# Kernel optimization log

Measured on AMD Instinct MI355X. Metric: run time of the kernel, lower is better.

## Reference

```python
import jax, jax.numpy as jnp
import numpy as np

N = 4096          # rank / n
OFF_DIAG = 4      # banded half-width
D_IN = 4096       # v: [N, D_IN]
D_OUT = 4096      # u: [D_OUT, N]
BATCH, SEQ = 4, 2048


def _banded_indices(n, off_diag):
    """All (row, col) entries of the 2*off_diag+1 diagonals, like torch.sparse.spdiags."""
    rows, cols = [], []
    for off in range(-off_diag, off_diag + 1):
        if off >= 0:
            i = np.arange(0, n - off)
        else:
            i = np.arange(-off, n)
        rows.append(i)
        cols.append(i + off)
    return np.concatenate(rows).astype(np.int32), np.concatenate(cols).astype(np.int32)


def setup_inputs() -> dict:
    key = jax.random.key(0)
    k_x, k_u, k_v, k_sp, k_s = jax.random.split(key, 5)
    row, col = _banded_indices(N, OFF_DIAG)
    nnz = row.shape[0]  # 36844
    return {
        "x": jax.random.normal(k_x, (BATCH, SEQ, D_IN), dtype=jnp.float32),
        "u": jax.random.normal(k_u, (D_OUT, N), dtype=jnp.float32),
        "v": jax.random.normal(k_v, (N, D_IN), dtype=jnp.float32),
        "s_pre": jax.random.uniform(k_sp, (N,), dtype=jnp.float32),  # singular values (diag)
        # kaiming_normal_ on a [1, nnz] tensor -> std = sqrt(2 / nnz)
        "s": jax.random.normal(k_s, (nnz,), dtype=jnp.float32) * np.float32(np.sqrt(2.0 / nnz)),
        "gate": jnp.zeros((1,), dtype=jnp.float32),
        "row": jnp.asarray(row),
        "col": jnp.asarray(col),
    }


def reference(x, u, v, s_pre, s, gate, row, col):
    n = s_pre.shape[0]
    # del_s = diag(s_pre) + scatter(s * sigmoid(gate)) at banded indices  -> [n, n]
    vals = s * jax.nn.sigmoid(gate)          # [nnz]
    M = jnp.zeros((n, n), dtype=x.dtype).at[row, col].add(vals)
    M = M.at[jnp.arange(n), jnp.arange(n)].add(s_pre)
    # weight = ((del_s @ v).T) @ u.T  -> [D_IN, D_OUT]
    weight = (M @ v).T @ u.T
    return x @ weight
```

## Files before the change

kernel.cpp:

```cpp
#include <hip/hip_runtime.h>
#include <cstdint>

typedef unsigned short u16;
typedef __attribute__((ext_vector_type(8))) __bf16 bf16x8;
typedef __attribute__((ext_vector_type(4))) float f32x4;

#define N_DIM 4096

__device__ __forceinline__ u16 f2bf(float f) {
    union { float f; unsigned u; } c; c.f = f;
    unsigned u = c.u;
    u += 0x7FFFu + ((u >> 16) & 1u);
    return (u16)(u >> 16);
}

__device__ __forceinline__ void gl_lds16(const u16* g, u16* l) {
    __builtin_amdgcn_global_load_lds(
        (const __attribute__((address_space(1))) void*)g,
        (__attribute__((address_space(3))) void*)l, 16, 0, 0);
}

__global__ void band_kernel(const float* __restrict__ s,
                            const float* __restrict__ s_pre,
                            const float* __restrict__ gate,
                            float* __restrict__ bnd) {
    int n = blockIdx.x * blockDim.x + threadIdx.x;
    if (n >= N_DIM) return;
    float sig = 1.0f / (1.0f + __expf(-gate[0]));
    const int base[9] = {0, 4092, 8185, 12279, 16374, 20470, 24565, 28659, 32752};
    #pragma unroll
    for (int o = 0; o < 9; ++o) {
        int off = o - 4;
        int col = n + off;
        float val = 0.0f;
        if (col >= 0 && col < N_DIM) {
            int idx = (off >= 0) ? (base[o] + n) : (base[o] + n + off);
            val = s[idx] * sig;
        }
        if (off == 0) val += s_pre[n];
        bnd[n * 9 + o] = val;
    }
}

__global__ void band_combine_t(const float* __restrict__ v,
                               const float* __restrict__ bnd,
                               u16* __restrict__ P) {
    __shared__ float tile[32][33];
    int n0 = blockIdx.x * 32;
    int d0 = blockIdx.y * 32;
    int tx = threadIdx.x;
    int ty = threadIdx.y;
    #pragma unroll
    for (int i = 0; i < 4; ++i) {
        int nl = ty + 8 * i;
        int n = n0 + nl;
        int d = d0 + tx;
        float acc = 0.0f;
        #pragma unroll
        for (int o = 0; o < 9; ++o) {
            int src = n + o - 4;
            float w = bnd[n * 9 + o];
            float vv = ((unsigned)src < (unsigned)N_DIM) ? v[(size_t)src * N_DIM + d] : 0.0f;
            acc += w * vv;
        }
        tile[nl][tx] = acc;
    }
    __syncthreads();
    #pragma unroll
    for (int i = 0; i < 4; ++i) {
        int dl = ty + 8 * i;
        P[(size_t)(d0 + dl) * N_DIM + (n0 + tx)] = f2bf(tile[tx][dl]);
    }
}

__global__ void cvt_bf16(const float* __restrict__ in, u16* __restrict__ out, int nElem4) {
    int i = blockIdx.x * blockDim.x + threadIdx.x;
    if (i >= nElem4) return;
    float4 f = ((const float4*)in)[i];
    ushort4 o;
    o.x = f2bf(f.x); o.y = f2bf(f.y); o.z = f2bf(f.z); o.w = f2bf(f.w);
    ((ushort4*)out)[i] = o;
}

#define BARRIER() __builtin_amdgcn_s_barrier()
#define LGKM0()   asm volatile("s_waitcnt lgkmcnt(0)" ::: "memory")
#define VMC(n)    asm volatile("s_waitcnt vmcnt(" #n ")" ::: "memory")

#define MFMA_Q(QM, QN) do {                                                   \
    __builtin_amdgcn_s_setprio(1);                                            \
    _Pragma("unroll")                                                         \
    for (int k_ = 0; k_ < 2; ++k_)                                            \
      _Pragma("unroll")                                                       \
      for (int i_ = 0; i_ < 4; ++i_)                                          \
        _Pragma("unroll")                                                     \
        for (int j_ = 0; j_ < 2; ++j_)                                        \
          acc[(QM)*4 + i_][(QN)*2 + j_] =                                     \
            __builtin_amdgcn_mfma_f32_16x16x32_bf16(                          \
              aR[i_][k_], bR[(QN)*2 + j_][k_],                                \
              acc[(QM)*4 + i_][(QN)*2 + j_], 0, 0, 0);                        \
    __builtin_amdgcn_s_setprio(0);                                            \
  } while (0)

template <bool OUT_BF16>
__global__ __launch_bounds__(512, 2)
void gemm_tn8(const u16* __restrict__ A, const u16* __restrict__ B,
              float* __restrict__ Cf, u16* __restrict__ Cb,
              int M, int N, int K) {
    __shared__ __align__(16) u16 As[2][16384];
    __shared__ __align__(16) u16 Bs[2][16384];

    const int tid = threadIdx.x;
    const int l   = tid & 63;
    const int w   = tid >> 6;
    const int wm  = w >> 2;
    const int wn  = w & 3;

    const int nbx = gridDim.x;
    const int nwg = nbx * gridDim.y;
    int lid = blockIdx.y * nbx + blockIdx.x;
    if ((nwg & 7) == 0) lid = (lid & 7) * (nwg >> 3) + (lid >> 3);
    const long m0 = (long)(lid / nbx) * 256;
    const long n0 = (long)(lid % nbx) * 256;

    const u16* Ab = A + m0 * (long)K;
    const u16* Bb = B + n0 * (long)K;

    const int lin16 = (l < 32) ? l : (l ^ 2);
    const int sr = lin16 >> 2;
    const int sc = (lin16 & 3) * 8;
    const int s0 = w;
    const int s1 = 8 + w;
    const int g0 = ((s0 >> 1) * 16 + sr) * K + (s0 & 1) * 32 + sc;
    const int g1 = ((s1 >> 1) * 16 + sr) * K + (s1 & 1) * 32 + sc;
    const int d0 = s0 * 512 + l * 8;
    const int d1 = s1 * 512 + l * 8;

    const int foff = (((((l & 15) << 6) + ((l >> 4) << 4)) ^ (((l >> 3) & 1) << 5)) >> 1);
    const int abase = wm * 8192;
    const int bbase = wn * 4096;

    f32x4 acc[8][4];
    #pragma unroll
    for (int i = 0; i < 8; ++i)
        #pragma unroll
        for (int j = 0; j < 4; ++j)
            acc[i][j] = (f32x4){0.f, 0.f, 0.f, 0.f};

    bf16x8 aR[4][2], bR[4][2];

    auto stageA = [&](int buf, int t, int h) {
        const u16* g = Ab + (long)h * 128 * K + (long)t * 64;
        u16* lb = &As[buf][h * 8192];
        gl_lds16(g + g0, lb + d0);
        gl_lds16(g + g1, lb + d1);
    };
    auto stageB = [&](int buf, int t, int h) {
        const u16* g = Bb + (long)h * 128 * K + (long)t * 64;
        u16* lb = &Bs[buf][h * 8192];
        gl_lds16(g + g0, lb + d0);
        gl_lds16(g + g1, lb + d1);
    };
    auto loadA4 = [&](int buf, int fmBase) {
        #pragma unroll
        for (int i = 0; i < 4; ++i)
            #pragma unroll
            for (int ks = 0; ks < 2; ++ks)
                aR[i][ks] = *(const bf16x8*)&As[buf][abase + (fmBase + i) * 1024 + ks * 512 + foff];
    };
    auto loadB2 = [&](int buf, int fnBase) {
        #pragma unroll
        for (int i = 0; i < 2; ++i)
            #pragma unroll
            for (int ks = 0; ks < 2; ++ks)
                bR[fnBase + i][ks] = *(const bf16x8*)&Bs[buf][bbase + (fnBase + i) * 1024 + ks * 512 + foff];
    };

    const int NT = K >> 6;

    stageA(0, 0, 0); stageA(0, 0, 1);
    stageB(0, 0, 0); stageB(0, 0, 1);
    stageB(1, 1, 0); stageB(1, 1, 1);
    VMC(4);
    BARRIER();

    for (int it = 0; it < (NT >> 1); ++it) {
        const int kt = it * 2;
        const int t2 = (kt + 2 < NT) ? kt + 2 : NT - 1;
        const int t3 = (kt + 3 < NT) ? kt + 3 : NT - 1;

        loadA4(0, 0); loadB2(0, 0);
        stageA(1, kt + 1, 0);
        BARRIER(); LGKM0();
        MFMA_Q(0, 0);
        BARRIER();

        loadB2(0, 2);
        stageA(1, kt + 1, 1);
        BARRIER(); LGKM0();
        MFMA_Q(0, 1);
        BARRIER();

        loadA4(0, 4);
        stageB(0, t2, 0);
        BARRIER(); LGKM0();
        MFMA_Q(1, 0);
        BARRIER();

        stageB(0, t2, 1);
        VMC(4);
        BARRIER(); LGKM0();
        MFMA_Q(1, 1);
        BARRIER();

        loadA4(1, 0); loadB2(1, 0);
        stageA(0, t2, 0);
        BARRIER(); LGKM0();
        MFMA_Q(0, 0);
        BARRIER();

        loadB2(1, 2);
        stageA(0, t2, 1);
        BARRIER(); LGKM0();
        MFMA_Q(0, 1);
        BARRIER();

        loadA4(1, 4);
        stageB(1, t3, 0);
        BARRIER(); LGKM0();
        MFMA_Q(1, 0);
        BARRIER();

        stageB(1, t3, 1);
        VMC(4);
        BARRIER(); LGKM0();
        MFMA_Q(1, 1);
        BARRIER();
    }

    VMC(0);

    const int cn = l & 15;
    const int rg = l >> 4;
    #pragma unroll
    for (int fm = 0; fm < 8; ++fm) {
        #pragma unroll
        for (int fn = 0; fn < 4; ++fn) {
            const long mb = m0 + wm * 128 + fm * 16 + rg * 4;
            const long nn = n0 + wn * 64 + fn * 16 + cn;
            #pragma unroll
            for (int r = 0; r < 4; ++r) {
                const long off = (mb + r) * N + nn;
                if (OUT_BF16) Cb[off] = f2bf(acc[fm][fn][r]);
                else          Cf[off] = acc[fm][fn][r];
            }
        }
    }
}

extern "C" void kernel_launch(void* const* d_in, const int* in_sizes, int n_in,
                              void* d_out, int out_size, void* d_ws, size_t ws_size,
                              hipStream_t stream) {
    const float* x     = (const float*)d_in[0];
    const float* u     = (const float*)d_in[1];
    const float* v     = (const float*)d_in[2];
    const float* s_pre = (const float*)d_in[3];
    const float* s     = (const float*)d_in[4];
    const float* gate  = (const float*)d_in[5];
    float* out = (float*)d_out;

    const int BS = 8192;
    const size_t NN = (size_t)N_DIM * N_DIM;

    char* ws = (char*)d_ws;
    float* bnd = (float*)ws;
    u16*   P   = (u16*)(ws + (1 << 18));
    u16*   Ubf = (u16*)(ws + (1 << 18) + NN * 2);
    u16*   Wt  = (u16*)(ws + (1 << 18) + NN * 4);
    u16*   Xbf = (u16*)(ws + (1 << 18) + NN * 6);

    band_kernel<<<16, 256, 0, stream>>>(s, s_pre, gate, bnd);

    band_combine_t<<<dim3(128, 128), dim3(32, 8), 0, stream>>>(v, bnd, P);

    cvt_bf16<<<(int)(NN / 4 / 256), 256, 0, stream>>>(u, Ubf, (int)(NN / 4));
    cvt_bf16<<<(int)((size_t)BS * N_DIM / 4 / 256), 256, 0, stream>>>(
        x, Xbf, (int)((size_t)BS * N_DIM / 4));

    gemm_tn8<true><<<dim3(N_DIM / 256, N_DIM / 256), 512, 0, stream>>>(
        Ubf, P, nullptr, Wt, N_DIM, N_DIM, N_DIM);

    gemm_tn8<false><<<dim3(N_DIM / 256, BS / 256), 512, 0, stream>>>(
        Xbf, Wt, out, nullptr, BS, N_DIM, N_DIM);
}
```

Baseline: 739.9 us.

## Double-buffer LDS fragment registers to overlap LDS reads with MFMA

Splits the A and B register fragments into Lo/Hi halves so the LDS reads for the next MFMA quadrant are issued while the current quadrant's MFMAs run. The explicit lgkmcnt(0) waits are dropped and the quadrant order is changed so each fragment is reused across two quadrants. The next tile's first fragments are prefetched before its MFMAs start. This is meant to hide LDS read latency behind matrix math, at the cost of more VGPRs and reliance on compiler-inserted waits for correctness.

```diff
diff --git a/kernel.cpp b/kernel.cpp
--- a/kernel.cpp
+++ b/kernel.cpp
@@ -83,10 +83,10 @@
 }
 
 #define BARRIER() __builtin_amdgcn_s_barrier()
-#define LGKM0()   asm volatile("s_waitcnt lgkmcnt(0)" ::: "memory")
+#define SCHEDB()  __builtin_amdgcn_sched_barrier(0)
 #define VMC(n)    asm volatile("s_waitcnt vmcnt(" #n ")" ::: "memory")
 
-#define MFMA_Q(QM, QN) do {                                                   \
+#define MFMA_Q(AH, BH, MB, NB) do {                                           \
     __builtin_amdgcn_s_setprio(1);                                            \
     _Pragma("unroll")                                                         \
     for (int k_ = 0; k_ < 2; ++k_)                                            \
@@ -94,10 +94,10 @@
       for (int i_ = 0; i_ < 4; ++i_)                                          \
         _Pragma("unroll")                                                     \
         for (int j_ = 0; j_ < 2; ++j_)                                        \
-          acc[(QM)*4 + i_][(QN)*2 + j_] =                                     \
+          acc[(MB) + i_][(NB) + j_] =                                         \
             __builtin_amdgcn_mfma_f32_16x16x32_bf16(                          \
-              aR[i_][k_], bR[(QN)*2 + j_][k_],                                \
-              acc[(QM)*4 + i_][(QN)*2 + j_], 0, 0, 0);                        \
+              AH[i_][k_], BH[j_][k_],                                         \
+              acc[(MB) + i_][(NB) + j_], 0, 0, 0);                            \
     __builtin_amdgcn_s_setprio(0);                                            \
   } while (0)
 
@@ -146,7 +146,8 @@
         for (int j = 0; j < 4; ++j)
             acc[i][j] = (f32x4){0.f, 0.f, 0.f, 0.f};
 
-    bf16x8 aR[4][2], bR[4][2];
+    bf16x8 aLo[4][2], aHi[4][2];
+    bf16x8 bLo[2][2], bHi[2][2];
 
     auto stageA = [&](int buf, int t, int h) {
         const u16* g = Ab + (long)h * 128 * K + (long)t * 64;
@@ -160,19 +161,19 @@
         gl_lds16(g + g0, lb + d0);
         gl_lds16(g + g1, lb + d1);
     };
-    auto loadA4 = [&](int buf, int fmBase) {
+    auto readA = [&](int buf, int h, bf16x8 (*dst)[2]) {
         #pragma unroll
         for (int i = 0; i < 4; ++i)
             #pragma unroll
             for (int ks = 0; ks < 2; ++ks)
-                aR[i][ks] = *(const bf16x8*)&As[buf][abase + (fmBase + i) * 1024 + ks * 512 + foff];
+                dst[i][ks] = *(const bf16x8*)&As[buf][abase + (h * 4 + i) * 1024 + ks * 512 + foff];
     };
-    auto loadB2 = [&](int buf, int fnBase) {
+    auto readB = [&](int buf, int h, bf16x8 (*dst)[2]) {
         #pragma unroll
         for (int i = 0; i < 2; ++i)
             #pragma unroll
             for (int ks = 0; ks < 2; ++ks)
-                bR[fnBase + i][ks] = *(const bf16x8*)&Bs[buf][bbase + (fnBase + i) * 1024 + ks * 512 + foff];
+                dst[i][ks] = *(const bf16x8*)&Bs[buf][bbase + (h * 2 + i) * 1024 + ks * 512 + foff];
     };
 
     const int NT = K >> 6;
@@ -182,58 +183,64 @@
     stageB(1, 1, 0); stageB(1, 1, 1);
     VMC(4);
     BARRIER();
+    readA(0, 0, aLo);
+    readB(0, 0, bLo);
 
     for (int it = 0; it < (NT >> 1); ++it) {
         const int kt = it * 2;
         const int t2 = (kt + 2 < NT) ? kt + 2 : NT - 1;
         const int t3 = (kt + 3 < NT) ? kt + 3 : NT - 1;
 
-        loadA4(0, 0); loadB2(0, 0);
         stageA(1, kt + 1, 0);
-        BARRIER(); LGKM0();
-        MFMA_Q(0, 0);
-        BARRIER();
-
-        loadB2(0, 2);
+        BARRIER();
+        readA(0, 1, aHi);
+        MFMA_Q(aLo, bLo, 0, 0);
+        BARRIER();
+
         stageA(1, kt + 1, 1);
-        BARRIER(); LGKM0();
-        MFMA_Q(0, 1);
-        BARRIER();
-
-        loadA4(0, 4);
+        BARRIER();
+        readB(0, 1, bHi);
+        MFMA_Q(aHi, bLo, 4, 0);
+        BARRIER();
+
         stageB(0, t2, 0);
-        BARRIER(); LGKM0();
-        MFMA_Q(1, 0);
+        BARRIER();
+        MFMA_Q(aLo, bHi, 0, 2);
         BARRIER();
 
         stageB(0, t2, 1);
         VMC(4);
-        BARRIER(); LGKM0();
-        MFMA_Q(1, 1);
-        BARRIER();
-
-        loadA4(1, 0); loadB2(1, 0);
+        BARRIER();
+        SCHEDB();
+        readA(1, 0, aLo);
+        readB(1, 0, bLo);
+        MFMA_Q(aHi, bHi, 4, 2);
+        BARRIER();
+
         stageA(0, t2, 0);
-        BARRIER(); LGKM0();
-        MFMA_Q(0, 0);
-        BARRIER();
-
-        loadB2(1, 2);
+        BARRIER();
+        readA(1, 1, aHi);
+        MFMA_Q(aLo, bLo, 0, 0);
+        BARRIER();
+
         stageA(0, t2, 1);
-        BARRIER(); LGKM0();
-        MFMA_Q(0, 1);
-        BARRIER();
-
-        loadA4(1, 4);
+        BARRIER();
+        readB(1, 1, bHi);
+        MFMA_Q(aHi, bLo, 4, 0);
+        BARRIER();
+
         stageB(1, t3, 0);
-        BARRIER(); LGKM0();
-        MFMA_Q(1, 0);
+        BARRIER();
+        MFMA_Q(aLo, bHi, 0, 2);
         BARRIER();
 
         stageB(1, t3, 1);
         VMC(4);
-        BARRIER(); LGKM0();
-        MFMA_Q(1, 1);
+        BARRIER();
+        SCHEDB();
+        readA(0, 0, aLo);
+        readB(0, 0, bLo);
+        MFMA_Q(aHi, bHi, 4, 2);
         BARRIER();
     }
 
```

New measurement: 764.2 us. 3.3% more time.
